# Kernel tuning notes

Measured on AMD Instinct MI355X. Metric: run time of the kernel, lower is better.

Reference implementation:

```python
import jax, jax.numpy as jnp
import numpy as np

R, S, N, D_IN, D_OUT = 4, 8, 4096, 64, 64


def prelu(v, alpha):
    # torch.nn.PReLU with a single learnable slope (default init 0.25)
    return jnp.where(v >= 0, v, alpha * v)


def setup_inputs() -> dict:
    key = jax.random.key(0)
    ks = jax.random.split(key, 6)
    theta = jax.random.uniform(ks[0], (R, S), dtype=jnp.float32)
    t = jax.random.uniform(ks[1], (R, S), dtype=jnp.float32)
    a = jax.random.uniform(ks[2], (R, N, N), dtype=jnp.float32)
    x = jax.random.normal(ks[3], (R, N, D_IN), dtype=jnp.float32)
    # per-relation Linear(input_dim, output_dim): weight [out,in], bias [out]
    fc_w = jax.random.normal(ks[4], (R, D_OUT, D_IN), dtype=jnp.float32) * (1.0 / np.sqrt(D_IN))
    fc_b = jnp.zeros((R, D_OUT), dtype=jnp.float32)
    # Conv2d(R, R, kernel_size=1): weight [R,R,1,1] -> [R,R], bias [R]
    conv_w = jax.random.normal(ks[5], (R, R), dtype=jnp.float32) * (1.0 / np.sqrt(R))
    conv_b = jnp.zeros((R,), dtype=jnp.float32)
    alpha0 = jnp.array(0.25, dtype=jnp.float32)  # PReLU for per-relation activation
    alpha1 = jnp.array(0.25, dtype=jnp.float32)  # PReLU after 1x1 conv
    return dict(theta=theta, t=t, a=a, x=x, fc_w=fc_w, fc_b=fc_b,
                conv_w=conv_w, conv_b=conv_b, alpha0=alpha0, alpha1=alpha1)


def reference(theta, t, a, x, fc_w, fc_b, conv_w, conv_b, alpha0, alpha1):
    # sum_step theta[r,s]*t[r,s]*a[r] == (sum_s theta[r,s]*t[r,s]) * a[r]
    coef = jnp.sum(theta * t, axis=-1)                               # [R]
    # diffusion: scaled dense matmul per relation (scale after matmul to avoid
    # materializing a scaled copy of the NxN matrix)
    feat = coef[:, None, None] * jnp.einsum('rij,rjd->rid', a, x)    # [R,N,D_IN]
    # per-relation Linear + PReLU
    diffusions = prelu(jnp.einsum('rnd,rod->rno', feat, fc_w) + fc_b[:, None, :], alpha0)  # [R,N,D_OUT]
    # 1x1 Conv2d over relation channels + PReLU
    latent = prelu(jnp.einsum('sr,rno->sno', conv_w, diffusions) + conv_b[:, None, None], alpha1)
    return (latent, diffusions)
```

## Files before the change

### kernel.cpp

```cpp
#include <hip/hip_runtime.h>

#define R_ 4
#define S_ 8
#define N_ 4096
#define D_ 64
#define KS_ 128
#define NST_ (N_ / KS_)

typedef __attribute__((ext_vector_type(8))) short bf16x8;
typedef __attribute__((ext_vector_type(4))) float f32x4;

__device__ __forceinline__ unsigned int f2bf(float f) {
    unsigned int u = __float_as_uint(f);
    return (u + 0x7FFFu + ((u >> 16) & 1u)) >> 16;
}

__global__ __launch_bounds__(256) void prep_kernel(
    const float* __restrict__ theta, const float* __restrict__ tt,
    const float* __restrict__ x, const float* __restrict__ fc_w,
    unsigned short* __restrict__ ycombT) {
    int r  = blockIdx.x >> 6;
    int kb = blockIdx.x & 63;
    int tid = threadIdx.x;

    __shared__ float xs[64][64];
    __shared__ float ws[64][65];

    const float* xp = x    + ((size_t)r * N_ + (size_t)kb * 64) * D_;
    const float* wp = fc_w + (size_t)r * D_ * D_;
    for (int i = 0; i < 16; ++i) {
        int flat = i * 256 + tid;
        xs[flat >> 6][flat & 63] = xp[flat];
        ws[flat >> 6][flat & 63] = wp[flat];
    }
    float coef = 0.f;
#pragma unroll
    for (int s = 0; s < S_; ++s) coef += theta[r * S_ + s] * tt[r * S_ + s];
    __syncthreads();

    int o = tid & 63, kg = tid >> 6;
    for (int kl = kg; kl < 64; kl += 4) {
        float dot = 0.f;
#pragma unroll
        for (int d = 0; d < D_; ++d) dot += xs[kl][d] * ws[o][d];
        ycombT[(size_t)(r * D_ + o) * N_ + (size_t)kb * 64 + kl] =
            (unsigned short)f2bf(coef * dot);
    }
}

__global__ __launch_bounds__(512) void gemm_kernel(
    const float* __restrict__ a, const unsigned short* __restrict__ ycombT,
    const float* __restrict__ fc_b, const float* __restrict__ alpha0p,
    float* __restrict__ out) {
    int bid = blockIdx.x;
    int r   = bid & 3;
    int rb  = bid >> 2;
    int tid  = threadIdx.x;
    int wave = tid >> 6;
    int wm   = wave & 3;
    int wk   = wave >> 2;
    int lane = tid & 63;
    int l15  = lane & 15;
    int kg   = lane >> 4;

    __shared__ __align__(16) char pool[65536];
#define ABASE(buf) ((buf) * 16384)
#define BBASE(buf) (32768 + (buf) * 16384)

    int arow_loc = tid >> 5;
    int ak       = (tid & 31) * 4;
    int agran    = (tid & 31) >> 1;
    int ahalf    = tid & 1;
    int swzA     = (arow_loc & 7) << 1;
    const float* asrc = a + ((size_t)(r * N_ + rb * 64)) * N_;

    int srow = tid >> 3, g2 = (tid & 7) * 2;
    int swzB = (srow & 7) << 1;
    const unsigned short* ysrc = ycombT + (size_t)(r * D_ + srow) * N_ + g2 * 8;

    int swzr = (l15 & 7) << 1;

    f32x4 acc0 = {0.f, 0.f, 0.f, 0.f};
    f32x4 acc1 = {0.f, 0.f, 0.f, 0.f};
    f32x4 acc2 = {0.f, 0.f, 0.f, 0.f};
    f32x4 acc3 = {0.f, 0.f, 0.f, 0.f};

    float4 an[4];
    uint4  bv0, bv1;

    auto loadA = [&](int s) {
#pragma unroll
        for (int j = 0; j < 4; ++j)
            an[j] = *(const float4*)(asrc + (size_t)(j * 16 + arow_loc) * N_
                                          + (size_t)s * KS_ + ak);
    };
    auto loadB = [&](int s) {
        bv0 = *(const uint4*)(ysrc + (size_t)s * KS_);
        bv1 = *(const uint4*)(ysrc + (size_t)s * KS_ + 8);
    };
    auto writeA = [&](int buf) {
#pragma unroll
        for (int j = 0; j < 4; ++j) {
            int rowj = j * 16 + arow_loc;
            uint2 p;
            p.x = (f2bf(an[j].y) << 16) | f2bf(an[j].x);
            p.y = (f2bf(an[j].w) << 16) | f2bf(an[j].z);
            *(uint2*)(pool + ABASE(buf) + rowj * 256
                      + ((agran ^ swzA) << 4) + (ahalf << 3)) = p;
        }
    };
    auto writeB = [&](int buf) {
        *(uint4*)(pool + BBASE(buf) + srow * 256 + (((g2    ) ^ swzB) << 4)) = bv0;
        *(uint4*)(pool + BBASE(buf) + srow * 256 + (((g2 + 1) ^ swzB) << 4)) = bv1;
    };
    auto compute = [&](int buf) {
#pragma unroll
        for (int step = 0; step < 2; ++step) {
            int slot = (((wk * 8 + step * 4 + kg) ^ swzr)) << 4;
            bf16x8 af = *(const bf16x8*)(pool + ABASE(buf) + (wm * 16 + l15) * 256 + slot);
            bf16x8 b0 = *(const bf16x8*)(pool + BBASE(buf) + ( 0 + l15) * 256 + slot);
            bf16x8 b1 = *(const bf16x8*)(pool + BBASE(buf) + (16 + l15) * 256 + slot);
            bf16x8 b2 = *(const bf16x8*)(pool + BBASE(buf) + (32 + l15) * 256 + slot);
            bf16x8 b3 = *(const bf16x8*)(pool + BBASE(buf) + (48 + l15) * 256 + slot);
            acc0 = __builtin_amdgcn_mfma_f32_16x16x32_bf16(af, b0, acc0, 0, 0, 0);
            acc1 = __builtin_amdgcn_mfma_f32_16x16x32_bf16(af, b1, acc1, 0, 0, 0);
            acc2 = __builtin_amdgcn_mfma_f32_16x16x32_bf16(af, b2, acc2, 0, 0, 0);
            acc3 = __builtin_amdgcn_mfma_f32_16x16x32_bf16(af, b3, acc3, 0, 0, 0);
        }
    };

    loadA(0); loadB(0);
    writeA(0); writeB(0);
    loadA(1); loadB(1);
    __syncthreads();

#pragma unroll 2
    for (int s = 0; s < NST_; ++s) {
        int buf = s & 1;
        compute(buf);
        __syncthreads();
        if (s + 1 < NST_) {
            writeA(buf ^ 1); writeB(buf ^ 1);
            if (s + 2 < NST_) { loadA(s + 2); loadB(s + 2); }
            __syncthreads();
        }
    }

    float (*red)[16][65] = (float (*)[16][65])pool;
    if (wk == 1) {
#pragma unroll
        for (int c = 0; c < 4; ++c) {
            f32x4 acc = (c == 0) ? acc0 : (c == 1) ? acc1 : (c == 2) ? acc2 : acc3;
#pragma unroll
            for (int j = 0; j < 4; ++j)
                red[wm][kg * 4 + j][c * 16 + l15] = acc[j];
        }
    }
    __syncthreads();
    if (wk == 0) {
        const float alpha0 = *alpha0p;
        const size_t diff_off = (size_t)R_ * N_ * D_;
#pragma unroll
        for (int c = 0; c < 4; ++c) {
            f32x4 acc = (c == 0) ? acc0 : (c == 1) ? acc1 : (c == 2) ? acc2 : acc3;
            int col = c * 16 + l15;
            float b = fc_b[r * D_ + col];
#pragma unroll
            for (int j = 0; j < 4; ++j) {
                int rloc = kg * 4 + j;
                float v = acc[j] + red[wm][rloc][col] + b;
                v = (v >= 0.f) ? v : alpha0 * v;
                out[diff_off + ((size_t)(r * N_ + rb * 64 + wm * 16 + rloc)) * D_ + col] = v;
            }
        }
    }
}

__global__ __launch_bounds__(256) void conv_kernel(
    const float* __restrict__ conv_w, const float* __restrict__ conv_b,
    const float* __restrict__ alpha1p, float* __restrict__ out) {
    const size_t nd = (size_t)N_ * D_;
    const size_t diff_off = (size_t)R_ * nd;
    size_t i = ((size_t)blockIdx.x * 256 + threadIdx.x) * 4;

    float4 d0 = *(const float4*)(out + diff_off + 0 * nd + i);
    float4 d1 = *(const float4*)(out + diff_off + 1 * nd + i);
    float4 d2 = *(const float4*)(out + diff_off + 2 * nd + i);
    float4 d3 = *(const float4*)(out + diff_off + 3 * nd + i);
    const float alpha1 = *alpha1p;
#pragma unroll
    for (int s = 0; s < R_; ++s) {
        float w0 = conv_w[s * R_ + 0], w1 = conv_w[s * R_ + 1];
        float w2 = conv_w[s * R_ + 2], w3 = conv_w[s * R_ + 3];
        float cb = conv_b[s];
        float4 v;
        v.x = cb + w0 * d0.x + w1 * d1.x + w2 * d2.x + w3 * d3.x;
        v.y = cb + w0 * d0.y + w1 * d1.y + w2 * d2.y + w3 * d3.y;
        v.z = cb + w0 * d0.z + w1 * d1.z + w2 * d2.z + w3 * d3.z;
        v.w = cb + w0 * d0.w + w1 * d1.w + w2 * d2.w + w3 * d3.w;
        v.x = (v.x >= 0.f) ? v.x : alpha1 * v.x;
        v.y = (v.y >= 0.f) ? v.y : alpha1 * v.y;
        v.z = (v.z >= 0.f) ? v.z : alpha1 * v.z;
        v.w = (v.w >= 0.f) ? v.w : alpha1 * v.w;
        *(float4*)(out + s * nd + i) = v;
    }
}

extern "C" void kernel_launch(void* const* d_in, const int* in_sizes, int n_in,
                              void* d_out, int out_size, void* d_ws, size_t ws_size,
                              hipStream_t stream) {
    const float* theta  = (const float*)d_in[0];
    const float* tt     = (const float*)d_in[1];
    const float* a      = (const float*)d_in[2];
    const float* x      = (const float*)d_in[3];
    const float* fc_w   = (const float*)d_in[4];
    const float* fc_b   = (const float*)d_in[5];
    const float* conv_w = (const float*)d_in[6];
    const float* conv_b = (const float*)d_in[7];
    const float* alpha0 = (const float*)d_in[8];
    const float* alpha1 = (const float*)d_in[9];
    float* out = (float*)d_out;
    unsigned short* ycombT = (unsigned short*)d_ws;

    prep_kernel<<<dim3(R_ * (N_ / 64)), dim3(256), 0, stream>>>(theta, tt, x, fc_w, ycombT);
    gemm_kernel<<<dim3((N_ / 64) * R_), dim3(512), 0, stream>>>(a, ycombT, fc_b, alpha0, out);
    conv_kernel<<<dim3((N_ * D_) / 4 / 256), dim3(256), 0, stream>>>(conv_w, conv_b, alpha1, out);
}
```

Measured before the change: 59.37 us.

## Split GEMM K dimension across blocks and fuse partial-sum combine with conv

Replaces the per-block intra-block split-K (two wave groups reduced through shared memory) with an inter-block split-K. Each block now covers 128 rows over half of K, with every wave owning 16 rows and a 64-wide K stage. Partial sums are written to a workspace, and a combine kernel adds the two halves, applies bias and PReLU, writes diffusions, then does the 1x1 conv, all in one pass. This removes the conv kernel's reread of diffusions and reduces LDS per block, aiming for better occupancy. The cost is extra global traffic for the partial buffers.

After: 79.81 us. 34.4% more time.

```diff
diff --git a/kernel.cpp b/kernel.cpp
--- a/kernel.cpp
+++ b/kernel.cpp
@@ -4,8 +4,10 @@
 #define S_ 8
 #define N_ 4096
 #define D_ 64
-#define KS_ 128
-#define NST_ (N_ / KS_)
+#define KS_ 64
+#define KH_ 2048
+#define NST_ (KH_ / KS_)
+#define PART_ELEMS ((size_t)2 * R_ * N_ * D_)
 
 typedef __attribute__((ext_vector_type(8))) short bf16x8;
 typedef __attribute__((ext_vector_type(4))) float f32x4;
@@ -48,37 +50,34 @@
     }
 }
 
-__global__ __launch_bounds__(512) void gemm_kernel(
+__global__ __launch_bounds__(512, 4) void gemm_kernel(
     const float* __restrict__ a, const unsigned short* __restrict__ ycombT,
-    const float* __restrict__ fc_b, const float* __restrict__ alpha0p,
-    float* __restrict__ out) {
+    float* __restrict__ part) {
     int bid = blockIdx.x;
     int r   = bid & 3;
-    int rb  = bid >> 2;
+    int q   = (bid >> 2) & 1;
+    int rg  = bid >> 3;
     int tid  = threadIdx.x;
     int wave = tid >> 6;
-    int wm   = wave & 3;
-    int wk   = wave >> 2;
     int lane = tid & 63;
     int l15  = lane & 15;
     int kg   = lane >> 4;
 
-    __shared__ __align__(16) char pool[65536];
+    __shared__ __align__(16) char pool[49152];
 #define ABASE(buf) ((buf) * 16384)
-#define BBASE(buf) (32768 + (buf) * 16384)
-
-    int arow_loc = tid >> 5;
-    int ak       = (tid & 31) * 4;
-    int agran    = (tid & 31) >> 1;
-    int ahalf    = tid & 1;
-    int swzA     = (arow_loc & 7) << 1;
-    const float* asrc = a + ((size_t)(r * N_ + rb * 64)) * N_;
-
-    int srow = tid >> 3, g2 = (tid & 7) * 2;
-    int swzB = (srow & 7) << 1;
-    const unsigned short* ysrc = ycombT + (size_t)(r * D_ + srow) * N_ + g2 * 8;
-
-    int swzr = (l15 & 7) << 1;
+#define BBASE(buf) (32768 + (buf) * 8192)
+
+    int arow0 = tid >> 4;
+    int ak    = (tid & 15) * 4;
+    int agran = (tid & 15) >> 1;
+    int ahalf = tid & 1;
+    int swzA  = arow0 & 7;
+    const float* asrc = a + ((size_t)(r * N_ + rg * 128)) * N_ + (size_t)q * KH_;
+
+    int brow = tid >> 3, bg = tid & 7;
+    const unsigned short* ysrc = ycombT + (size_t)(r * D_ + brow) * N_
+                                 + (size_t)q * KH_ + bg * 8;
+    int bslot = (bg ^ (brow & 7)) << 4;
 
     f32x4 acc0 = {0.f, 0.f, 0.f, 0.f};
     f32x4 acc1 = {0.f, 0.f, 0.f, 0.f};
@@ -86,42 +85,40 @@
     f32x4 acc3 = {0.f, 0.f, 0.f, 0.f};
 
     float4 an[4];
-    uint4  bv0, bv1;
+    uint4  bv;
 
     auto loadA = [&](int s) {
 #pragma unroll
         for (int j = 0; j < 4; ++j)
-            an[j] = *(const float4*)(asrc + (size_t)(j * 16 + arow_loc) * N_
+            an[j] = *(const float4*)(asrc + (size_t)(arow0 + 32 * j) * N_
                                           + (size_t)s * KS_ + ak);
     };
     auto loadB = [&](int s) {
-        bv0 = *(const uint4*)(ysrc + (size_t)s * KS_);
-        bv1 = *(const uint4*)(ysrc + (size_t)s * KS_ + 8);
+        bv = *(const uint4*)(ysrc + (size_t)s * KS_);
     };
     auto writeA = [&](int buf) {
 #pragma unroll
         for (int j = 0; j < 4; ++j) {
-            int rowj = j * 16 + arow_loc;
+            int row = arow0 + 32 * j;
             uint2 p;
             p.x = (f2bf(an[j].y) << 16) | f2bf(an[j].x);
             p.y = (f2bf(an[j].w) << 16) | f2bf(an[j].z);
-            *(uint2*)(pool + ABASE(buf) + rowj * 256
+            *(uint2*)(pool + ABASE(buf) + row * 128
                       + ((agran ^ swzA) << 4) + (ahalf << 3)) = p;
         }
     };
     auto writeB = [&](int buf) {
-        *(uint4*)(pool + BBASE(buf) + srow * 256 + (((g2    ) ^ swzB) << 4)) = bv0;
-        *(uint4*)(pool + BBASE(buf) + srow * 256 + (((g2 + 1) ^ swzB) << 4)) = bv1;
+        *(uint4*)(pool + BBASE(buf) + brow * 128 + bslot) = bv;
     };
     auto compute = [&](int buf) {
 #pragma unroll
-        for (int step = 0; step < 2; ++step) {
-            int slot = (((wk * 8 + step * 4 + kg) ^ swzr)) << 4;
-            bf16x8 af = *(const bf16x8*)(pool + ABASE(buf) + (wm * 16 + l15) * 256 + slot);
-            bf16x8 b0 = *(const bf16x8*)(pool + BBASE(buf) + ( 0 + l15) * 256 + slot);
-            bf16x8 b1 = *(const bf16x8*)(pool + BBASE(buf) + (16 + l15) * 256 + slot);
-            bf16x8 b2 = *(const bf16x8*)(pool + BBASE(buf) + (32 + l15) * 256 + slot);
-            bf16x8 b3 = *(const bf16x8*)(pool + BBASE(buf) + (48 + l15) * 256 + slot);
+        for (int ks = 0; ks < 2; ++ks) {
+            int slot = ((ks * 4 + kg) ^ (l15 & 7)) << 4;
+            bf16x8 af = *(const bf16x8*)(pool + ABASE(buf) + (wave * 16 + l15) * 128 + slot);
+            bf16x8 b0 = *(const bf16x8*)(pool + BBASE(buf) + ( 0 + l15) * 128 + slot);
+            bf16x8 b1 = *(const bf16x8*)(pool + BBASE(buf) + (16 + l15) * 128 + slot);
+            bf16x8 b2 = *(const bf16x8*)(pool + BBASE(buf) + (32 + l15) * 128 + slot);
+            bf16x8 b3 = *(const bf16x8*)(pool + BBASE(buf) + (48 + l15) * 128 + slot);
             acc0 = __builtin_amdgcn_mfma_f32_16x16x32_bf16(af, b0, acc0, 0, 0, 0);
             acc1 = __builtin_amdgcn_mfma_f32_16x16x32_bf16(af, b1, acc1, 0, 0, 0);
             acc2 = __builtin_amdgcn_mfma_f32_16x16x32_bf16(af, b2, acc2, 0, 0, 0);
@@ -146,63 +143,60 @@
         }
     }
 
-    float (*red)[16][65] = (float (*)[16][65])pool;
-    if (wk == 1) {
-#pragma unroll
-        for (int c = 0; c < 4; ++c) {
-            f32x4 acc = (c == 0) ? acc0 : (c == 1) ? acc1 : (c == 2) ? acc2 : acc3;
-#pragma unroll
-            for (int j = 0; j < 4; ++j)
-                red[wm][kg * 4 + j][c * 16 + l15] = acc[j];
-        }
-    }
-    __syncthreads();
-    if (wk == 0) {
-        const float alpha0 = *alpha0p;
-        const size_t diff_off = (size_t)R_ * N_ * D_;
-#pragma unroll
-        for (int c = 0; c < 4; ++c) {
-            f32x4 acc = (c == 0) ? acc0 : (c == 1) ? acc1 : (c == 2) ? acc2 : acc3;
-            int col = c * 16 + l15;
-            float b = fc_b[r * D_ + col];
-#pragma unroll
-            for (int j = 0; j < 4; ++j) {
-                int rloc = kg * 4 + j;
-                float v = acc[j] + red[wm][rloc][col] + b;
-                v = (v >= 0.f) ? v : alpha0 * v;
-                out[diff_off + ((size_t)(r * N_ + rb * 64 + wm * 16 + rloc)) * D_ + col] = v;
-            }
-        }
-    }
-}
-
-__global__ __launch_bounds__(256) void conv_kernel(
+    float* pb = part + (((size_t)(q * R_ + r) * N_) + rg * 128 + wave * 16) * D_;
+#pragma unroll
+    for (int c = 0; c < 4; ++c) {
+        f32x4 acc = (c == 0) ? acc0 : (c == 1) ? acc1 : (c == 2) ? acc2 : acc3;
+#pragma unroll
+        for (int j = 0; j < 4; ++j)
+            pb[(size_t)(kg * 4 + j) * D_ + c * 16 + l15] = acc[j];
+    }
+}
+
+__global__ __launch_bounds__(256) void combine_kernel(
+    const float* __restrict__ part, const float* __restrict__ fc_b,
     const float* __restrict__ conv_w, const float* __restrict__ conv_b,
-    const float* __restrict__ alpha1p, float* __restrict__ out) {
+    const float* __restrict__ alpha0p, const float* __restrict__ alpha1p,
+    float* __restrict__ out) {
     const size_t nd = (size_t)N_ * D_;
     const size_t diff_off = (size_t)R_ * nd;
     size_t i = ((size_t)blockIdx.x * 256 + threadIdx.x) * 4;
-
-    float4 d0 = *(const float4*)(out + diff_off + 0 * nd + i);
-    float4 d1 = *(const float4*)(out + diff_off + 1 * nd + i);
-    float4 d2 = *(const float4*)(out + diff_off + 2 * nd + i);
-    float4 d3 = *(const float4*)(out + diff_off + 3 * nd + i);
-    const float alpha1 = *alpha1p;
-#pragma unroll
-    for (int s = 0; s < R_; ++s) {
-        float w0 = conv_w[s * R_ + 0], w1 = conv_w[s * R_ + 1];
-        float w2 = conv_w[s * R_ + 2], w3 = conv_w[s * R_ + 3];
-        float cb = conv_b[s];
+    int col0 = (int)(i & 63);
+    const float alpha0 = *alpha0p, alpha1 = *alpha1p;
+
+    float4 diff[4];
+#pragma unroll
+    for (int r = 0; r < R_; ++r) {
+        float4 p0 = *(const float4*)(part + (size_t)(0 * R_ + r) * nd + i);
+        float4 p1 = *(const float4*)(part + (size_t)(1 * R_ + r) * nd + i);
+        float4 b  = *(const float4*)(fc_b + r * D_ + col0);
+        float4 s;
+        s.x = p0.x + p1.x + b.x;
+        s.y = p0.y + p1.y + b.y;
+        s.z = p0.z + p1.z + b.z;
+        s.w = p0.w + p1.w + b.w;
+        s.x = (s.x >= 0.f) ? s.x : alpha0 * s.x;
+        s.y = (s.y >= 0.f) ? s.y : alpha0 * s.y;
+        s.z = (s.z >= 0.f) ? s.z : alpha0 * s.z;
+        s.w = (s.w >= 0.f) ? s.w : alpha0 * s.w;
+        diff[r] = s;
+        *(float4*)(out + diff_off + r * nd + i) = s;
+    }
+#pragma unroll
+    for (int sx = 0; sx < R_; ++sx) {
+        float w0 = conv_w[sx * R_ + 0], w1 = conv_w[sx * R_ + 1];
+        float w2 = conv_w[sx * R_ + 2], w3 = conv_w[sx * R_ + 3];
+        float cb = conv_b[sx];
         float4 v;
-        v.x = cb + w0 * d0.x + w1 * d1.x + w2 * d2.x + w3 * d3.x;
-        v.y = cb + w0 * d0.y + w1 * d1.y + w2 * d2.y + w3 * d3.y;
-        v.z = cb + w0 * d0.z + w1 * d1.z + w2 * d2.z + w3 * d3.z;
-        v.w = cb + w0 * d0.w + w1 * d1.w + w2 * d2.w + w3 * d3.w;
+        v.x = cb + w0 * diff[0].x + w1 * diff[1].x + w2 * diff[2].x + w3 * diff[3].x;
+        v.y = cb + w0 * diff[0].y + w1 * diff[1].y + w2 * diff[2].y + w3 * diff[3].y;
+        v.z = cb + w0 * diff[0].z + w1 * diff[1].z + w2 * diff[2].z + w3 * diff[3].z;
+        v.w = cb + w0 * diff[0].w + w1 * diff[1].w + w2 * diff[2].w + w3 * diff[3].w;
         v.x = (v.x >= 0.f) ? v.x : alpha1 * v.x;
         v.y = (v.y >= 0.f) ? v.y : alpha1 * v.y;
         v.z = (v.z >= 0.f) ? v.z : alpha1 * v.z;
         v.w = (v.w >= 0.f) ? v.w : alpha1 * v.w;
-        *(float4*)(out + s * nd + i) = v;
+        *(float4*)(out + sx * nd + i) = v;
     }
 }
 
@@ -220,9 +214,13 @@
     const float* alpha0 = (const float*)d_in[8];
     const float* alpha1 = (const float*)d_in[9];
     float* out = (float*)d_out;
-    unsigned short* ycombT = (unsigned short*)d_ws;
+
+    float* part = (float*)d_ws;
+    unsigned short* ycombT =
+        (unsigned short*)((char*)d_ws + PART_ELEMS * sizeof(float));
 
     prep_kernel<<<dim3(R_ * (N_ / 64)), dim3(256), 0, stream>>>(theta, tt, x, fc_w, ycombT);
-    gemm_kernel<<<dim3((N_ / 64) * R_), dim3(512), 0, stream>>>(a, ycombT, fc_b, alpha0, out);
-    conv_kernel<<<dim3((N_ * D_) / 4 / 256), dim3(256), 0, stream>>>(conv_w, conv_b, alpha1, out);
-}
+    gemm_kernel<<<dim3(256), dim3(512), 0, stream>>>(a, ycombT, part);
+    combine_kernel<<<dim3((N_ * D_) / 4 / 256), dim3(256), 0, stream>>>(
+        part, fc_b, conv_w, conv_b, alpha0, alpha1, out);
+}
```

## Double K-tile to 256 with single-buffered LDS and row-per-wave A loads

Applied to the files above, without the earlier changes.

Doubles the K-step per iteration to 256 elements and drops the double-buffered LDS scheme in favour of a single A/B buffer. Each wave now loads whole 1KB row segments of the fp32 adjacency matrix, and the XOR swizzle is widened to match. The intent is to halve the number of barrier-separated iterations and keep more global loads in flight per thread. The cost is more live registers for the prefetch arrays, and the loss of LDS double buffering means writes must wait for compute to finish.

Result: slower. 92.31 us (+55.5%).

```diff
diff --git a/kernel.cpp b/kernel.cpp
--- a/kernel.cpp
+++ b/kernel.cpp
@@ -4,7 +4,7 @@
 #define S_ 8
 #define N_ 4096
 #define D_ 64
-#define KS_ 128
+#define KS_ 256
 #define NST_ (N_ / KS_)
 
 typedef __attribute__((ext_vector_type(8))) short bf16x8;
@@ -64,64 +64,63 @@
     int kg   = lane >> 4;
 
     __shared__ __align__(16) char pool[65536];
-#define ABASE(buf) ((buf) * 16384)
-#define BBASE(buf) (32768 + (buf) * 16384)
-
-    int arow_loc = tid >> 5;
-    int ak       = (tid & 31) * 4;
-    int agran    = (tid & 31) >> 1;
-    int ahalf    = tid & 1;
-    int swzA     = (arow_loc & 7) << 1;
+#define BBASE 32768
+
+    int ak    = (lane) * 4;
+    int agran = lane >> 1;
+    int ahalf = lane & 1;
+    int swzA  = (wave & 7) << 2;
     const float* asrc = a + ((size_t)(r * N_ + rb * 64)) * N_;
 
-    int srow = tid >> 3, g2 = (tid & 7) * 2;
-    int swzB = (srow & 7) << 1;
-    const unsigned short* ysrc = ycombT + (size_t)(r * D_ + srow) * N_ + g2 * 8;
-
-    int swzr = (l15 & 7) << 1;
+    int brow = tid >> 3, bg0 = tid & 7;
+    const unsigned short* ysrc = ycombT + (size_t)(r * D_ + brow) * N_;
+    int swzB = (brow & 7) << 2;
+
+    int swzr = (l15 & 7) << 2;
 
     f32x4 acc0 = {0.f, 0.f, 0.f, 0.f};
     f32x4 acc1 = {0.f, 0.f, 0.f, 0.f};
     f32x4 acc2 = {0.f, 0.f, 0.f, 0.f};
     f32x4 acc3 = {0.f, 0.f, 0.f, 0.f};
 
-    float4 an[4];
-    uint4  bv0, bv1;
+    float4 an[8];
+    uint4  bv[4];
 
     auto loadA = [&](int s) {
 #pragma unroll
-        for (int j = 0; j < 4; ++j)
-            an[j] = *(const float4*)(asrc + (size_t)(j * 16 + arow_loc) * N_
+        for (int j = 0; j < 8; ++j)
+            an[j] = *(const float4*)(asrc + (size_t)(8 * j + wave) * N_
                                           + (size_t)s * KS_ + ak);
     };
     auto loadB = [&](int s) {
-        bv0 = *(const uint4*)(ysrc + (size_t)s * KS_);
-        bv1 = *(const uint4*)(ysrc + (size_t)s * KS_ + 8);
-    };
-    auto writeA = [&](int buf) {
-#pragma unroll
-        for (int j = 0; j < 4; ++j) {
-            int rowj = j * 16 + arow_loc;
+#pragma unroll
+        for (int jj = 0; jj < 4; ++jj)
+            bv[jj] = *(const uint4*)(ysrc + (size_t)s * KS_ + (bg0 + 8 * jj) * 8);
+    };
+    auto writeA = [&]() {
+#pragma unroll
+        for (int j = 0; j < 8; ++j) {
+            int row = 8 * j + wave;
             uint2 p;
             p.x = (f2bf(an[j].y) << 16) | f2bf(an[j].x);
             p.y = (f2bf(an[j].w) << 16) | f2bf(an[j].z);
-            *(uint2*)(pool + ABASE(buf) + rowj * 256
-                      + ((agran ^ swzA) << 4) + (ahalf << 3)) = p;
-        }
-    };
-    auto writeB = [&](int buf) {
-        *(uint4*)(pool + BBASE(buf) + srow * 256 + (((g2    ) ^ swzB) << 4)) = bv0;
-        *(uint4*)(pool + BBASE(buf) + srow * 256 + (((g2 + 1) ^ swzB) << 4)) = bv1;
-    };
-    auto compute = [&](int buf) {
-#pragma unroll
-        for (int step = 0; step < 2; ++step) {
-            int slot = (((wk * 8 + step * 4 + kg) ^ swzr)) << 4;
-            bf16x8 af = *(const bf16x8*)(pool + ABASE(buf) + (wm * 16 + l15) * 256 + slot);
-            bf16x8 b0 = *(const bf16x8*)(pool + BBASE(buf) + ( 0 + l15) * 256 + slot);
-            bf16x8 b1 = *(const bf16x8*)(pool + BBASE(buf) + (16 + l15) * 256 + slot);
-            bf16x8 b2 = *(const bf16x8*)(pool + BBASE(buf) + (32 + l15) * 256 + slot);
-            bf16x8 b3 = *(const bf16x8*)(pool + BBASE(buf) + (48 + l15) * 256 + slot);
+            *(uint2*)(pool + row * 512 + ((agran ^ swzA) << 4) + (ahalf << 3)) = p;
+        }
+    };
+    auto writeB = [&]() {
+#pragma unroll
+        for (int jj = 0; jj < 4; ++jj)
+            *(uint4*)(pool + BBASE + brow * 512 + (((bg0 + 8 * jj) ^ swzB) << 4)) = bv[jj];
+    };
+    auto compute = [&]() {
+#pragma unroll
+        for (int st = 0; st < 4; ++st) {
+            int slot = ((wk * 16 + st * 4 + kg) ^ swzr) << 4;
+            bf16x8 af = *(const bf16x8*)(pool + (wm * 16 + l15) * 512 + slot);
+            bf16x8 b0 = *(const bf16x8*)(pool + BBASE + ( 0 + l15) * 512 + slot);
+            bf16x8 b1 = *(const bf16x8*)(pool + BBASE + (16 + l15) * 512 + slot);
+            bf16x8 b2 = *(const bf16x8*)(pool + BBASE + (32 + l15) * 512 + slot);
+            bf16x8 b3 = *(const bf16x8*)(pool + BBASE + (48 + l15) * 512 + slot);
             acc0 = __builtin_amdgcn_mfma_f32_16x16x32_bf16(af, b0, acc0, 0, 0, 0);
             acc1 = __builtin_amdgcn_mfma_f32_16x16x32_bf16(af, b1, acc1, 0, 0, 0);
             acc2 = __builtin_amdgcn_mfma_f32_16x16x32_bf16(af, b2, acc2, 0, 0, 0);
@@ -130,17 +129,15 @@
     };
 
     loadA(0); loadB(0);
-    writeA(0); writeB(0);
+    writeA(); writeB();
     loadA(1); loadB(1);
     __syncthreads();
 
-#pragma unroll 2
     for (int s = 0; s < NST_; ++s) {
-        int buf = s & 1;
-        compute(buf);
+        compute();
         __syncthreads();
         if (s + 1 < NST_) {
-            writeA(buf ^ 1); writeB(buf ^ 1);
+            writeA(); writeB();
             if (s + 2 < NST_) { loadA(s + 2); loadB(s + 2); }
             __syncthreads();
         }
```
